# Optimization experiments

Hardware: AMD Instinct MI355X
Metric: run time of the kernel (lower is better)

The kernel has to match this reference:

```python
import jax, jax.numpy as jnp
import numpy as np

D = 256
H = 4
HD = D // H


def setup_inputs() -> dict:
    key = jax.random.key(0)
    ks = jax.random.split(key, 12)
    A, T = 64, 512
    s = 1.0 / np.sqrt(D)
    return {
        "features": jax.random.normal(ks[0], (A, T, D), jnp.float32),
        "positions": jax.random.normal(ks[1], (A, T, 2), jnp.float32),
        "Wq": jax.random.normal(ks[2], (D, D), jnp.float32) * s,
        "bq": jnp.zeros((D,), jnp.float32),
        "Wk": jax.random.normal(ks[3], (D, D), jnp.float32) * s,
        "bk": jnp.zeros((D,), jnp.float32),
        "Wv": jax.random.normal(ks[4], (D, D), jnp.float32) * s,
        "bv": jnp.zeros((D,), jnp.float32),
        "Wo": jax.random.normal(ks[5], (D, D), jnp.float32) * s,
        "bo": jnp.zeros((D,), jnp.float32),
        "max_distance": 2,
        "time_window": 64,
    }


def _sparse_mask(positions, max_distance, time_window):
    # positions: [A, T, 2] -> allowed [A, T, T]
    A, T, _ = positions.shape
    diff = positions[:, :, None, :] - positions[:, None, :, :]  # [A,T,T,2]
    dist2 = jnp.sum(diff * diff, axis=-1)                       # [A,T,T]
    t = jnp.arange(T)
    tmask = jnp.abs(t[:, None] - t[None, :]) <= time_window      # [T,T]
    return (dist2 <= float(max_distance) ** 2) & tmask[None]     # [A,T,T]


def reference(features, positions, Wq, bq, Wk, bk, Wv, bv, Wo, bo,
              max_distance, time_window):
    A, T, Dm = features.shape
    allowed = _sparse_mask(positions, max_distance, time_window)  # [A,T,T]
    q = features @ Wq.T + bq
    k = features @ Wk.T + bk
    v = features @ Wv.T + bv
    # split heads: [A, T, H, HD]
    q = q.reshape(A, T, H, HD)
    k = k.reshape(A, T, H, HD)
    v = v.reshape(A, T, H, HD)
    scale = 1.0 / np.sqrt(HD)
    scores = jnp.einsum("athd,ashd->ahts", q, k) * scale          # [A,H,T,T]
    scores = jnp.where(allowed[:, None], scores, -jnp.inf)
    attn = jax.nn.softmax(scores, axis=-1)
    out = jnp.einsum("ahts,ashd->athd", attn, v).reshape(A, T, Dm)
    return out @ Wo.T + bo
```

## Files before the change

### kernel.cpp

```cpp
#include <hip/hip_runtime.h>
#include <hip/hip_bf16.h>
#include <cstdint>
#include <cstddef>

typedef __attribute__((ext_vector_type(8))) _Float16 half8;
typedef __attribute__((ext_vector_type(4))) float floatx4;

#define MFMA16(a, b, c) __builtin_amdgcn_mfma_f32_16x16x32_f16((a), (b), (c), 0, 0, 0)

#define GLOAD_LDS16(g, l)                                                     \
    __builtin_amdgcn_global_load_lds(                                         \
        (const __attribute__((address_space(1))) void*)(g),                   \
        (__attribute__((address_space(3))) void*)(l), 16, 0, 0)

#define NFEAT 8388608

__global__ __launch_bounds__(256) void qkv_fused(
    const float* __restrict__ feat,
    const float* __restrict__ Wq, const float* __restrict__ Wk,
    const float* __restrict__ Wv,
    const float* __restrict__ bq, const float* __restrict__ bk,
    const float* __restrict__ bv,
    _Float16* __restrict__ Qb, _Float16* __restrict__ Kb, _Float16* __restrict__ Vb)
{
    __shared__ _Float16 Xs[4 * 128 * 64];
    __shared__ _Float16 Ws[128 * 64];

    const int n   = blockIdx.x;
    const int idx = n >> 3;
    const int bm  = (n & 7) * 32 + (idx >> 1);
    const int bn  = idx & 1;

    const int tid  = threadIdx.x;
    const int lane = tid & 63, wid = tid >> 6;
    const int quad = lane >> 4, l16 = lane & 15;
    const int wm = wid & 1, wn = wid >> 1;

    const float* Xg = feat + (size_t)bm * 128 * 256;
#pragma unroll
    for (int sl = 0; sl < 4; ++sl)
#pragma unroll
        for (int i = 0; i < 4; ++i) {
            int g   = tid + 256 * i;
            int row = g >> 3, chd = g & 7;
            int chs = chd ^ (row & 7);
            const float* s = Xg + (size_t)row * 256 + sl * 64 + chs * 8;
            float4 v0 = *(const float4*)s;
            float4 v1 = *(const float4*)(s + 4);
            half8 h = { (_Float16)v0.x, (_Float16)v0.y, (_Float16)v0.z, (_Float16)v0.w,
                        (_Float16)v1.x, (_Float16)v1.y, (_Float16)v1.z, (_Float16)v1.w };
            *(half8*)(&Xs[sl * 8192 + row * 64 + chd * 8]) = h;
        }

    const float* Wz[3] = { Wq, Wk, Wv };
    const float* bz[3] = { bq, bk, bv };
    _Float16*    oz[3] = { Qb, Kb, Vb };

    int wrow[4], wchd[4];
#pragma unroll
    for (int i = 0; i < 4; ++i) {
        int g = tid + 256 * i;
        wrow[i] = g >> 3;
        wchd[i] = g & 7;
    }
    float4 pv0[4], pv1[4];

    auto loadW = [&](int t) {
        const float* base = Wz[t >> 2] + (size_t)bn * 32768 + (t & 3) * 64;
#pragma unroll
        for (int i = 0; i < 4; ++i) {
            int chs = wchd[i] ^ (wrow[i] & 7);
            const float* s = base + (size_t)wrow[i] * 256 + chs * 8;
            pv0[i] = *(const float4*)s;
            pv1[i] = *(const float4*)(s + 4);
        }
    };
    auto storeW = [&]() {
#pragma unroll
        for (int i = 0; i < 4; ++i) {
            half8 h = { (_Float16)pv0[i].x, (_Float16)pv0[i].y,
                        (_Float16)pv0[i].z, (_Float16)pv0[i].w,
                        (_Float16)pv1[i].x, (_Float16)pv1[i].y,
                        (_Float16)pv1[i].z, (_Float16)pv1[i].w };
            *(half8*)(&Ws[wrow[i] * 64 + wchd[i] * 8]) = h;
        }
    };

    loadW(0);
    storeW();
    floatx4 acc[4][4] = {};

#pragma unroll 1
    for (int t = 0; t < 12; ++t) {
        __syncthreads();
        if (t < 11) loadW(t + 1);
        const int ks = t & 3;
#pragma unroll
        for (int kh = 0; kh < 2; ++kh) {
            half8 af[4], bf[4];
#pragma unroll
            for (int mi = 0; mi < 4; ++mi) {
                int row = wm * 64 + mi * 16 + l16;
                int cs  = (kh * 4 + quad) ^ (row & 7);
                af[mi] = *(const half8*)(&Xs[ks * 8192 + row * 64 + cs * 8]);
            }
#pragma unroll
            for (int ni = 0; ni < 4; ++ni) {
                int row = wn * 64 + ni * 16 + l16;
                int cs  = (kh * 4 + quad) ^ (row & 7);
                bf[ni] = *(const half8*)(&Ws[row * 64 + cs * 8]);
            }
#pragma unroll
            for (int mi = 0; mi < 4; ++mi)
#pragma unroll
                for (int ni = 0; ni < 4; ++ni)
                    acc[mi][ni] = MFMA16(af[mi], bf[ni], acc[mi][ni]);
        }
        __syncthreads();
        if (t < 11) storeW();
        if ((t & 3) == 3) {
            const int z = t >> 2;
            const float* bias = bz[z];
            _Float16*    outp = oz[z];
#pragma unroll
            for (int ni = 0; ni < 4; ++ni) {
                int col = bn * 128 + wn * 64 + ni * 16 + l16;
                float bv2 = bias[col];
#pragma unroll
                for (int mi = 0; mi < 4; ++mi) {
#pragma unroll
                    for (int r = 0; r < 4; ++r) {
                        int row = bm * 128 + wm * 64 + mi * 16 + quad * 4 + r;
                        outp[(size_t)row * 256 + col] =
                            (_Float16)(acc[mi][ni][r] + bv2);
                    }
                    acc[mi][ni] = floatx4{0.f, 0.f, 0.f, 0.f};
                }
            }
        }
    }
}

__global__ __launch_bounds__(256) void out_gemm(
    const _Float16* __restrict__ attnH, const float* __restrict__ Wo,
    const float* __restrict__ bo, float* __restrict__ out)
{
    __shared__ _Float16 Xs[4 * 128 * 64];
    __shared__ _Float16 Ws[128 * 64];

    const int n   = blockIdx.x;
    const int idx = n >> 3;
    const int bm  = (n & 7) * 32 + (idx >> 1);
    const int bn  = idx & 1;

    const int tid  = threadIdx.x;
    const int lane = tid & 63, wid = tid >> 6;
    const int quad = lane >> 4, l16 = lane & 15;
    const int wm = wid & 1, wn = wid >> 1;

    const _Float16* Ag = attnH + (size_t)bm * 128 * 256;
#pragma unroll
    for (int sl = 0; sl < 4; ++sl)
#pragma unroll
        for (int i = 0; i < 4; ++i) {
            int grp = wid * 4 + i;
            int row = grp * 8 + (lane >> 3);
            int sc  = (lane & 7) ^ (row & 7);
            GLOAD_LDS16(Ag + (size_t)row * 256 + sl * 64 + sc * 8,
                        Xs + sl * 8192 + grp * 512);
        }

    int wrow[4], wchd[4];
#pragma unroll
    for (int i = 0; i < 4; ++i) {
        int g = tid + 256 * i;
        wrow[i] = g >> 3;
        wchd[i] = g & 7;
    }
    float4 pv0[4], pv1[4];

    auto loadW = [&](int t) {
        const float* base = Wo + (size_t)bn * 32768 + t * 64;
#pragma unroll
        for (int i = 0; i < 4; ++i) {
            int chs = wchd[i] ^ (wrow[i] & 7);
            const float* s = base + (size_t)wrow[i] * 256 + chs * 8;
            pv0[i] = *(const float4*)s;
            pv1[i] = *(const float4*)(s + 4);
        }
    };
    auto storeW = [&]() {
#pragma unroll
        for (int i = 0; i < 4; ++i) {
            half8 h = { (_Float16)pv0[i].x, (_Float16)pv0[i].y,
                        (_Float16)pv0[i].z, (_Float16)pv0[i].w,
                        (_Float16)pv1[i].x, (_Float16)pv1[i].y,
                        (_Float16)pv1[i].z, (_Float16)pv1[i].w };
            *(half8*)(&Ws[wrow[i] * 64 + wchd[i] * 8]) = h;
        }
    };

    loadW(0);
    storeW();
    floatx4 acc[4][4] = {};

#pragma unroll 1
    for (int t = 0; t < 4; ++t) {
        __syncthreads();
        if (t < 3) loadW(t + 1);
#pragma unroll
        for (int kh = 0; kh < 2; ++kh) {
            half8 af[4], bf[4];
#pragma unroll
            for (int mi = 0; mi < 4; ++mi) {
                int row = wm * 64 + mi * 16 + l16;
                int cs  = (kh * 4 + quad) ^ (row & 7);
                af[mi] = *(const half8*)(&Xs[t * 8192 + row * 64 + cs * 8]);
            }
#pragma unroll
            for (int ni = 0; ni < 4; ++ni) {
                int row = wn * 64 + ni * 16 + l16;
                int cs  = (kh * 4 + quad) ^ (row & 7);
                bf[ni] = *(const half8*)(&Ws[row * 64 + cs * 8]);
            }
#pragma unroll
            for (int mi = 0; mi < 4; ++mi)
#pragma unroll
                for (int ni = 0; ni < 4; ++ni)
                    acc[mi][ni] = MFMA16(af[mi], bf[ni], acc[mi][ni]);
        }
        __syncthreads();
        if (t < 3) storeW();
    }

#pragma unroll
    for (int ni = 0; ni < 4; ++ni) {
        int col = bn * 128 + wn * 64 + ni * 16 + l16;
        float bv = bo[col];
#pragma unroll
        for (int mi = 0; mi < 4; ++mi)
#pragma unroll
            for (int r = 0; r < 4; ++r) {
                int row = bm * 128 + wm * 64 + mi * 16 + quad * 4 + r;
                out[(size_t)row * 256 + col] = acc[mi][ni][r] + bv;
            }
    }
}

__global__ __launch_bounds__(256) void attn_kernel(
    const _Float16* __restrict__ Qb, const _Float16* __restrict__ Kb,
    const _Float16* __restrict__ Vb, const float* __restrict__ positions,
    const int* __restrict__ mdp, const int* __restrict__ twp,
    _Float16* __restrict__ attnb)
{
    const int n   = blockIdx.x;
    const int idx = n >> 3;
    const int a   = (n & 7) * 8 + (idx >> 5);
    const int rem = idx & 31;
    const int qt  = rem >> 2, h = rem & 3;

    const int q0 = qt * 64;
    const int s_base = q0 - 64;
    const int tid = threadIdx.x, lane = tid & 63, wid = tid >> 6;
    const int quad = lane >> 4, l16 = lane & 15;

    __shared__ _Float16 KPs[192 * 64];
    __shared__ _Float16 Vt[64 * 192];

    const size_t abase = (size_t)a * 512;
    const int md = *mdp, tw = *twp;
    const float md2 = (float)(md * md);

    const size_t qrow = abase + q0 + wid * 16 + l16;
    half8 aq0 = *(const half8*)(Qb + qrow * 256 + h * 64 + quad * 8);
    half8 aq1 = *(const half8*)(Qb + qrow * 256 + h * 64 + 32 + quad * 8);
    float qpx[4], qpy[4];
    int trow[4];
#pragma unroll
    for (int r = 0; r < 4; ++r) {
        int m = wid * 16 + quad * 4 + r;
        trow[r] = q0 + m;
        float2 qp = *(const float2*)(positions + (abase + q0 + m) * 2);
        qpx[r] = qp.x;
        qpy[r] = qp.y;
    }

#pragma unroll
    for (int i = 0; i < 6; ++i) {
        int grp = wid * 6 + i;
        int si  = grp * 8 + (lane >> 3);
        int sc  = min(max(s_base + si, 0), 511);
        int ch  = (lane & 7) ^ (si & 7);
        GLOAD_LDS16(Kb + (abase + sc) * 256 + h * 64 + ch * 8, KPs + grp * 512);
    }
#pragma unroll
    for (int i = 0; i < 3; ++i) {
        int g   = tid + 256 * i;
        int si2 = (g % 96) * 2;
        int d0  = (g / 96) * 8;
        int sa  = min(max(s_base + si2, 0), 511);
        int sb  = min(max(s_base + si2 + 1, 0), 511);
        half8 v0 = *(const half8*)(Vb + (abase + sa) * 256 + h * 64 + d0);
        half8 v1 = *(const half8*)(Vb + (abase + sb) * 256 + h * 64 + d0);
        int c = si2 >> 3;
#pragma unroll
        for (int j = 0; j < 8; ++j) {
            int d  = d0 + j;
            int cs = (c & ~7) | ((c & 7) ^ (d & 7));
            union { _Float16 hh[2]; uint32_t u; } p;
            p.hh[0] = v0[j]; p.hh[1] = v1[j];
            *(uint32_t*)(&Vt[d * 192 + cs * 8 + (si2 & 7)]) = p.u;
        }
    }
    __syncthreads();

    floatx4 S[12];
#pragma unroll
    for (int j = 0; j < 12; ++j) {
        int si = j * 16 + l16;
        half8 bk0 = *(const half8*)(&KPs[si * 64 + ((quad) ^ (si & 7)) * 8]);
        half8 bk1 = *(const half8*)(&KPs[si * 64 + ((4 + quad) ^ (si & 7)) * 8]);
        floatx4 acc = {};
        acc = MFMA16(aq0, bk0, acc);
        acc = MFMA16(aq1, bk1, acc);
        int sr = s_base + si;
        int sc = min(max(sr, 0), 511);
        float2 kp = *(const float2*)(positions + (abase + sc) * 2);
        bool svalid = (sr >= 0) && (sr < 512);
#pragma unroll
        for (int r = 0; r < 4; ++r) {
            float dx = qpx[r] - kp.x, dy = qpy[r] - kp.y;
            float d2 = dx * dx + dy * dy;
            int dt = trow[r] - sr; dt = dt < 0 ? -dt : dt;
            bool ok = svalid && (d2 <= md2) && (dt <= tw);
            S[j][r] = ok ? acc[r] * 0.125f : -1e30f;
        }
    }

    float minv[4];
#pragma unroll
    for (int r = 0; r < 4; ++r) {
        float m = -1e30f;
#pragma unroll
        for (int j = 0; j < 12; ++j) m = fmaxf(m, S[j][r]);
        m = fmaxf(m, __shfl_xor(m, 1));
        m = fmaxf(m, __shfl_xor(m, 2));
        m = fmaxf(m, __shfl_xor(m, 4));
        m = fmaxf(m, __shfl_xor(m, 8));
        float l = 0.f;
#pragma unroll
        for (int j = 0; j < 12; ++j) {
            float p = __expf(S[j][r] - m);
            S[j][r] = p;
            l += p;
        }
        l += __shfl_xor(l, 1);
        l += __shfl_xor(l, 2);
        l += __shfl_xor(l, 4);
        l += __shfl_xor(l, 8);
        minv[r] = 1.0f / l;
    }

    __syncthreads();

    _Float16* Ps = KPs + wid * (16 * 192);
#pragma unroll
    for (int j = 0; j < 12; ++j)
#pragma unroll
        for (int r = 0; r < 4; ++r) {
            int row = quad * 4 + r;
            int col = j * 16 + l16;
            int ch  = (col >> 3) ^ (row & 7);
            Ps[row * 192 + ch * 8 + (col & 7)] = (_Float16)(S[j][r] * minv[r]);
        }

    half8 af[6];
#pragma unroll
    for (int k = 0; k < 6; ++k) {
        int ch = (k * 4 + quad) ^ (l16 & 7);
        af[k] = *(const half8*)(&Ps[l16 * 192 + ch * 8]);
    }
#pragma unroll
    for (int nn = 0; nn < 4; ++nn) {
        floatx4 accO = {};
#pragma unroll
        for (int k = 0; k < 6; ++k) {
            int row = nn * 16 + l16;
            int c   = k * 4 + quad;
            int cs  = (c & ~7) | ((c & 7) ^ (row & 7));
            half8 bv = *(const half8*)(&Vt[row * 192 + cs * 8]);
            accO = MFMA16(af[k], bv, accO);
        }
#pragma unroll
        for (int r = 0; r < 4; ++r) {
            int row = q0 + wid * 16 + quad * 4 + r;
            attnb[(abase + row) * 256 + h * 64 + nn * 16 + l16] = (_Float16)accO[r];
        }
    }
}

extern "C" void kernel_launch(void* const* d_in, const int* in_sizes, int n_in,
                              void* d_out, int out_size, void* d_ws, size_t ws_size,
                              hipStream_t stream)
{
    const float* feat = (const float*)d_in[0];
    const float* pos  = (const float*)d_in[1];
    const float* Wq   = (const float*)d_in[2];
    const float* bq   = (const float*)d_in[3];
    const float* Wk   = (const float*)d_in[4];
    const float* bk   = (const float*)d_in[5];
    const float* Wv   = (const float*)d_in[6];
    const float* bv   = (const float*)d_in[7];
    const float* Wo   = (const float*)d_in[8];
    const float* bo   = (const float*)d_in[9];
    const int*   md   = (const int*)d_in[10];
    const int*   tw   = (const int*)d_in[11];
    float*       out  = (float*)d_out;

    _Float16* ws    = (_Float16*)d_ws;
    _Float16* Qb    = ws;
    _Float16* Kb    = Qb + NFEAT;
    _Float16* Vb    = Kb + NFEAT;
    _Float16* attnH = Vb + NFEAT;

    qkv_fused<<<512, 256, 0, stream>>>(feat, Wq, Wk, Wv, bq, bk, bv, Qb, Kb, Vb);

    attn_kernel<<<2048, 256, 0, stream>>>(Qb, Kb, Vb, pos, md, tw, attnH);

    out_gemm<<<512, 256, 0, stream>>>(attnH, Wo, bo, out);
}
```

Measured before the change: 170.1 us.

## Fuse attention with output projection and pre-convert inputs to fp16

```diff
diff --git a/kernel.cpp b/kernel.cpp
--- a/kernel.cpp
+++ b/kernel.cpp
@@ -4,6 +4,7 @@
 #include <cstddef>
 
 typedef __attribute__((ext_vector_type(8))) _Float16 half8;
+typedef __attribute__((ext_vector_type(4))) _Float16 half4v;
 typedef __attribute__((ext_vector_type(4))) float floatx4;
 
 #define MFMA16(a, b, c) __builtin_amdgcn_mfma_f32_16x16x32_f16((a), (b), (c), 0, 0, 0)
@@ -14,11 +15,32 @@
         (__attribute__((address_space(3))) void*)(l), 16, 0, 0)
 
 #define NFEAT 8388608
+#define NW    65536
+
+__global__ __launch_bounds__(256) void convert_kernel(
+    const float* __restrict__ feat, const float* __restrict__ wq,
+    const float* __restrict__ wk, const float* __restrict__ wv,
+    const float* __restrict__ wo, _Float16* __restrict__ out)
+{
+    long tid  = (long)blockIdx.x * blockDim.x + threadIdx.x;
+    long base = tid * 4;
+    if (base >= (long)NFEAT + 4L * NW) return;
+    const float* src;
+    long off;
+    if (base < NFEAT) { src = feat; off = base; }
+    else {
+        long r = base - NFEAT;
+        int  w = (int)(r >> 16);
+        off = r & (NW - 1);
+        src = (w == 0) ? wq : (w == 1) ? wk : (w == 2) ? wv : wo;
+    }
+    float4 v = *(const float4*)(src + off);
+    half4v h = { (_Float16)v.x, (_Float16)v.y, (_Float16)v.z, (_Float16)v.w };
+    *(half4v*)(out + base) = h;
+}
 
 __global__ __launch_bounds__(256) void qkv_fused(
-    const float* __restrict__ feat,
-    const float* __restrict__ Wq, const float* __restrict__ Wk,
-    const float* __restrict__ Wv,
+    const _Float16* __restrict__ featH, const _Float16* __restrict__ WH,
     const float* __restrict__ bq, const float* __restrict__ bk,
     const float* __restrict__ bv,
     _Float16* __restrict__ Qb, _Float16* __restrict__ Kb, _Float16* __restrict__ Vb)
@@ -36,23 +58,18 @@
     const int quad = lane >> 4, l16 = lane & 15;
     const int wm = wid & 1, wn = wid >> 1;
 
-    const float* Xg = feat + (size_t)bm * 128 * 256;
+    const _Float16* Xg = featH + (size_t)bm * 128 * 256;
 #pragma unroll
     for (int sl = 0; sl < 4; ++sl)
 #pragma unroll
         for (int i = 0; i < 4; ++i) {
-            int g   = tid + 256 * i;
-            int row = g >> 3, chd = g & 7;
-            int chs = chd ^ (row & 7);
-            const float* s = Xg + (size_t)row * 256 + sl * 64 + chs * 8;
-            float4 v0 = *(const float4*)s;
-            float4 v1 = *(const float4*)(s + 4);
-            half8 h = { (_Float16)v0.x, (_Float16)v0.y, (_Float16)v0.z, (_Float16)v0.w,
-                        (_Float16)v1.x, (_Float16)v1.y, (_Float16)v1.z, (_Float16)v1.w };
-            *(half8*)(&Xs[sl * 8192 + row * 64 + chd * 8]) = h;
-        }
-
-    const float* Wz[3] = { Wq, Wk, Wv };
+            int grp = wid * 4 + i;
+            int row = grp * 8 + (lane >> 3);
+            int sc  = (lane & 7) ^ (row & 7);
+            GLOAD_LDS16(Xg + (size_t)row * 256 + sl * 64 + sc * 8,
+                        Xs + sl * 8192 + grp * 512);
+        }
+
     const float* bz[3] = { bq, bk, bv };
     _Float16*    oz[3] = { Qb, Kb, Vb };
 
@@ -63,27 +80,21 @@
         wrow[i] = g >> 3;
         wchd[i] = g & 7;
     }
-    float4 pv0[4], pv1[4];
+    half8 pw[4];
 
     auto loadW = [&](int t) {
-        const float* base = Wz[t >> 2] + (size_t)bn * 32768 + (t & 3) * 64;
+        const _Float16* base = WH + (size_t)(t >> 2) * NW
+                             + (size_t)bn * 32768 + (t & 3) * 64;
 #pragma unroll
         for (int i = 0; i < 4; ++i) {
             int chs = wchd[i] ^ (wrow[i] & 7);
-            const float* s = base + (size_t)wrow[i] * 256 + chs * 8;
-            pv0[i] = *(const float4*)s;
-            pv1[i] = *(const float4*)(s + 4);
+            pw[i] = *(const half8*)(base + (size_t)wrow[i] * 256 + chs * 8);
         }
     };
     auto storeW = [&]() {
 #pragma unroll
-        for (int i = 0; i < 4; ++i) {
-            half8 h = { (_Float16)pv0[i].x, (_Float16)pv0[i].y,
-                        (_Float16)pv0[i].z, (_Float16)pv0[i].w,
-                        (_Float16)pv1[i].x, (_Float16)pv1[i].y,
-                        (_Float16)pv1[i].z, (_Float16)pv1[i].w };
-            *(half8*)(&Ws[wrow[i] * 64 + wchd[i] * 8]) = h;
-        }
+        for (int i = 0; i < 4; ++i)
+            *(half8*)(&Ws[wrow[i] * 64 + wchd[i] * 8]) = pw[i];
     };
 
     loadW(0);
@@ -141,139 +152,34 @@
     }
 }
 
-__global__ __launch_bounds__(256) void out_gemm(
-    const _Float16* __restrict__ attnH, const float* __restrict__ Wo,
-    const float* __restrict__ bo, float* __restrict__ out)
+__global__ __launch_bounds__(256) void attn_out(
+    const _Float16* __restrict__ Qb, const _Float16* __restrict__ Kb,
+    const _Float16* __restrict__ Vb, const _Float16* __restrict__ WoH,
+    const float* __restrict__ positions, const float* __restrict__ bo,
+    const int* __restrict__ mdp, const int* __restrict__ twp,
+    float* __restrict__ out)
 {
-    __shared__ _Float16 Xs[4 * 128 * 64];
-    __shared__ _Float16 Ws[128 * 64];
+    __shared__ _Float16 SH[24576];
+    __shared__ _Float16 Wos[16384];
+
+    _Float16* KPs = SH;
+    _Float16* Vt  = SH + 12288;
+    _Float16* Os  = SH;
 
     const int n   = blockIdx.x;
     const int idx = n >> 3;
-    const int bm  = (n & 7) * 32 + (idx >> 1);
-    const int bn  = idx & 1;
-
-    const int tid  = threadIdx.x;
-    const int lane = tid & 63, wid = tid >> 6;
-    const int quad = lane >> 4, l16 = lane & 15;
-    const int wm = wid & 1, wn = wid >> 1;
-
-    const _Float16* Ag = attnH + (size_t)bm * 128 * 256;
-#pragma unroll
-    for (int sl = 0; sl < 4; ++sl)
-#pragma unroll
-        for (int i = 0; i < 4; ++i) {
-            int grp = wid * 4 + i;
-            int row = grp * 8 + (lane >> 3);
-            int sc  = (lane & 7) ^ (row & 7);
-            GLOAD_LDS16(Ag + (size_t)row * 256 + sl * 64 + sc * 8,
-                        Xs + sl * 8192 + grp * 512);
-        }
-
-    int wrow[4], wchd[4];
-#pragma unroll
-    for (int i = 0; i < 4; ++i) {
-        int g = tid + 256 * i;
-        wrow[i] = g >> 3;
-        wchd[i] = g & 7;
-    }
-    float4 pv0[4], pv1[4];
-
-    auto loadW = [&](int t) {
-        const float* base = Wo + (size_t)bn * 32768 + t * 64;
-#pragma unroll
-        for (int i = 0; i < 4; ++i) {
-            int chs = wchd[i] ^ (wrow[i] & 7);
-            const float* s = base + (size_t)wrow[i] * 256 + chs * 8;
-            pv0[i] = *(const float4*)s;
-            pv1[i] = *(const float4*)(s + 4);
-        }
-    };
-    auto storeW = [&]() {
-#pragma unroll
-        for (int i = 0; i < 4; ++i) {
-            half8 h = { (_Float16)pv0[i].x, (_Float16)pv0[i].y,
-                        (_Float16)pv0[i].z, (_Float16)pv0[i].w,
-                        (_Float16)pv1[i].x, (_Float16)pv1[i].y,
-                        (_Float16)pv1[i].z, (_Float16)pv1[i].w };
-            *(half8*)(&Ws[wrow[i] * 64 + wchd[i] * 8]) = h;
-        }
-    };
-
-    loadW(0);
-    storeW();
-    floatx4 acc[4][4] = {};
-
-#pragma unroll 1
-    for (int t = 0; t < 4; ++t) {
-        __syncthreads();
-        if (t < 3) loadW(t + 1);
-#pragma unroll
-        for (int kh = 0; kh < 2; ++kh) {
-            half8 af[4], bf[4];
-#pragma unroll
-            for (int mi = 0; mi < 4; ++mi) {
-                int row = wm * 64 + mi * 16 + l16;
-                int cs  = (kh * 4 + quad) ^ (row & 7);
-                af[mi] = *(const half8*)(&Xs[t * 8192 + row * 64 + cs * 8]);
-            }
-#pragma unroll
-            for (int ni = 0; ni < 4; ++ni) {
-                int row = wn * 64 + ni * 16 + l16;
-                int cs  = (kh * 4 + quad) ^ (row & 7);
-                bf[ni] = *(const half8*)(&Ws[row * 64 + cs * 8]);
-            }
-#pragma unroll
-            for (int mi = 0; mi < 4; ++mi)
-#pragma unroll
-                for (int ni = 0; ni < 4; ++ni)
-                    acc[mi][ni] = MFMA16(af[mi], bf[ni], acc[mi][ni]);
-        }
-        __syncthreads();
-        if (t < 3) storeW();
-    }
-
-#pragma unroll
-    for (int ni = 0; ni < 4; ++ni) {
-        int col = bn * 128 + wn * 64 + ni * 16 + l16;
-        float bv = bo[col];
-#pragma unroll
-        for (int mi = 0; mi < 4; ++mi)
-#pragma unroll
-            for (int r = 0; r < 4; ++r) {
-                int row = bm * 128 + wm * 64 + mi * 16 + quad * 4 + r;
-                out[(size_t)row * 256 + col] = acc[mi][ni][r] + bv;
-            }
-    }
-}
-
-__global__ __launch_bounds__(256) void attn_kernel(
-    const _Float16* __restrict__ Qb, const _Float16* __restrict__ Kb,
-    const _Float16* __restrict__ Vb, const float* __restrict__ positions,
-    const int* __restrict__ mdp, const int* __restrict__ twp,
-    _Float16* __restrict__ attnb)
-{
-    const int n   = blockIdx.x;
-    const int idx = n >> 3;
-    const int a   = (n & 7) * 8 + (idx >> 5);
-    const int rem = idx & 31;
-    const int qt  = rem >> 2, h = rem & 3;
+    const int a   = (n & 7) * 8 + (idx >> 3);
+    const int qt  = idx & 7;
 
     const int q0 = qt * 64;
     const int s_base = q0 - 64;
     const int tid = threadIdx.x, lane = tid & 63, wid = tid >> 6;
     const int quad = lane >> 4, l16 = lane & 15;
 
-    __shared__ _Float16 KPs[192 * 64];
-    __shared__ _Float16 Vt[64 * 192];
-
     const size_t abase = (size_t)a * 512;
     const int md = *mdp, tw = *twp;
     const float md2 = (float)(md * md);
 
-    const size_t qrow = abase + q0 + wid * 16 + l16;
-    half8 aq0 = *(const half8*)(Qb + qrow * 256 + h * 64 + quad * 8);
-    half8 aq1 = *(const half8*)(Qb + qrow * 256 + h * 64 + 32 + quad * 8);
     float qpx[4], qpy[4];
     int trow[4];
 #pragma unroll
@@ -284,45 +190,10 @@
         qpx[r] = qp.x;
         qpy[r] = qp.y;
     }
-
-#pragma unroll
-    for (int i = 0; i < 6; ++i) {
-        int grp = wid * 6 + i;
-        int si  = grp * 8 + (lane >> 3);
-        int sc  = min(max(s_base + si, 0), 511);
-        int ch  = (lane & 7) ^ (si & 7);
-        GLOAD_LDS16(Kb + (abase + sc) * 256 + h * 64 + ch * 8, KPs + grp * 512);
-    }
-#pragma unroll
-    for (int i = 0; i < 3; ++i) {
-        int g   = tid + 256 * i;
-        int si2 = (g % 96) * 2;
-        int d0  = (g / 96) * 8;
-        int sa  = min(max(s_base + si2, 0), 511);
-        int sb  = min(max(s_base + si2 + 1, 0), 511);
-        half8 v0 = *(const half8*)(Vb + (abase + sa) * 256 + h * 64 + d0);
-        half8 v1 = *(const half8*)(Vb + (abase + sb) * 256 + h * 64 + d0);
-        int c = si2 >> 3;
-#pragma unroll
-        for (int j = 0; j < 8; ++j) {
-            int d  = d0 + j;
-            int cs = (c & ~7) | ((c & 7) ^ (d & 7));
-            union { _Float16 hh[2]; uint32_t u; } p;
-            p.hh[0] = v0[j]; p.hh[1] = v1[j];
-            *(uint32_t*)(&Vt[d * 192 + cs * 8 + (si2 & 7)]) = p.u;
-        }
-    }
-    __syncthreads();
-
-    floatx4 S[12];
+    uint64_t ok_bits = 0;
 #pragma unroll
     for (int j = 0; j < 12; ++j) {
         int si = j * 16 + l16;
-        half8 bk0 = *(const half8*)(&KPs[si * 64 + ((quad) ^ (si & 7)) * 8]);
-        half8 bk1 = *(const half8*)(&KPs[si * 64 + ((4 + quad) ^ (si & 7)) * 8]);
-        floatx4 acc = {};
-        acc = MFMA16(aq0, bk0, acc);
-        acc = MFMA16(aq1, bk1, acc);
         int sr = s_base + si;
         int sc = min(max(sr, 0), 511);
         float2 kp = *(const float2*)(positions + (abase + sc) * 2);
@@ -332,69 +203,174 @@
             float dx = qpx[r] - kp.x, dy = qpy[r] - kp.y;
             float d2 = dx * dx + dy * dy;
             int dt = trow[r] - sr; dt = dt < 0 ? -dt : dt;
-            bool ok = svalid && (d2 <= md2) && (dt <= tw);
-            S[j][r] = ok ? acc[r] * 0.125f : -1e30f;
-        }
-    }
-
-    float minv[4];
-#pragma unroll
-    for (int r = 0; r < 4; ++r) {
-        float m = -1e30f;
-#pragma unroll
-        for (int j = 0; j < 12; ++j) m = fmaxf(m, S[j][r]);
-        m = fmaxf(m, __shfl_xor(m, 1));
-        m = fmaxf(m, __shfl_xor(m, 2));
-        m = fmaxf(m, __shfl_xor(m, 4));
-        m = fmaxf(m, __shfl_xor(m, 8));
-        float l = 0.f;
+            if (svalid && (d2 <= md2) && (dt <= tw))
+                ok_bits |= (1ull << (j * 4 + r));
+        }
+    }
+
+    floatx4 accO[4][4] = {};
+
+#pragma unroll
+    for (int h = 0; h < 4; ++h) {
+#pragma unroll
+        for (int i = 0; i < 6; ++i) {
+            int grp = wid * 6 + i;
+            int si  = grp * 8 + (lane >> 3);
+            int sc  = min(max(s_base + si, 0), 511);
+            int ch  = (lane & 7) ^ (si & 7);
+            GLOAD_LDS16(Kb + (abase + sc) * 256 + h * 64 + ch * 8, KPs + grp * 512);
+        }
+#pragma unroll
+        for (int i = 0; i < 3; ++i) {
+            int g   = tid + 256 * i;
+            int si2 = (g % 96) * 2;
+            int d0  = (g / 96) * 8;
+            int sa  = min(max(s_base + si2, 0), 511);
+            int sb  = min(max(s_base + si2 + 1, 0), 511);
+            half8 v0 = *(const half8*)(Vb + (abase + sa) * 256 + h * 64 + d0);
+            half8 v1 = *(const half8*)(Vb + (abase + sb) * 256 + h * 64 + d0);
+            int c = si2 >> 3;
+#pragma unroll
+            for (int j = 0; j < 8; ++j) {
+                int d  = d0 + j;
+                int cs = (c & ~7) | ((c & 7) ^ (d & 7));
+                union { _Float16 hh[2]; uint32_t u; } p;
+                p.hh[0] = v0[j]; p.hh[1] = v1[j];
+                *(uint32_t*)(&Vt[d * 192 + cs * 8 + (si2 & 7)]) = p.u;
+            }
+        }
+        const size_t qrow = abase + q0 + wid * 16 + l16;
+        half8 aq0 = *(const half8*)(Qb + qrow * 256 + h * 64 + quad * 8);
+        half8 aq1 = *(const half8*)(Qb + qrow * 256 + h * 64 + 32 + quad * 8);
+        __syncthreads();
+
+        floatx4 S[12];
 #pragma unroll
         for (int j = 0; j < 12; ++j) {
-            float p = __expf(S[j][r] - m);
-            S[j][r] = p;
-            l += p;
-        }
-        l += __shfl_xor(l, 1);
-        l += __shfl_xor(l, 2);
-        l += __shfl_xor(l, 4);
-        l += __shfl_xor(l, 8);
-        minv[r] = 1.0f / l;
-    }
-
-    __syncthreads();
-
-    _Float16* Ps = KPs + wid * (16 * 192);
-#pragma unroll
-    for (int j = 0; j < 12; ++j)
+            int si = j * 16 + l16;
+            half8 bk0 = *(const half8*)(&KPs[si * 64 + ((quad) ^ (si & 7)) * 8]);
+            half8 bk1 = *(const half8*)(&KPs[si * 64 + ((4 + quad) ^ (si & 7)) * 8]);
+            floatx4 acc = {};
+            acc = MFMA16(aq0, bk0, acc);
+            acc = MFMA16(aq1, bk1, acc);
+#pragma unroll
+            for (int r = 0; r < 4; ++r) {
+                bool ok = (ok_bits >> (j * 4 + r)) & 1;
+                S[j][r] = ok ? acc[r] * 0.125f : -1e30f;
+            }
+        }
+
+        float minv[4];
 #pragma unroll
         for (int r = 0; r < 4; ++r) {
-            int row = quad * 4 + r;
-            int col = j * 16 + l16;
-            int ch  = (col >> 3) ^ (row & 7);
-            Ps[row * 192 + ch * 8 + (col & 7)] = (_Float16)(S[j][r] * minv[r]);
-        }
-
-    half8 af[6];
-#pragma unroll
-    for (int k = 0; k < 6; ++k) {
-        int ch = (k * 4 + quad) ^ (l16 & 7);
-        af[k] = *(const half8*)(&Ps[l16 * 192 + ch * 8]);
-    }
-#pragma unroll
-    for (int nn = 0; nn < 4; ++nn) {
-        floatx4 accO = {};
+            float m = -1e30f;
+#pragma unroll
+            for (int j = 0; j < 12; ++j) m = fmaxf(m, S[j][r]);
+            m = fmaxf(m, __shfl_xor(m, 1));
+            m = fmaxf(m, __shfl_xor(m, 2));
+            m = fmaxf(m, __shfl_xor(m, 4));
+            m = fmaxf(m, __shfl_xor(m, 8));
+            float l = 0.f;
+#pragma unroll
+            for (int j = 0; j < 12; ++j) {
+                float p = __expf(S[j][r] - m);
+                S[j][r] = p;
+                l += p;
+            }
+            l += __shfl_xor(l, 1);
+            l += __shfl_xor(l, 2);
+            l += __shfl_xor(l, 4);
+            l += __shfl_xor(l, 8);
+            minv[r] = 1.0f / l;
+        }
+
+        __syncthreads();
+
+        _Float16* Ps = KPs + wid * (16 * 192);
+#pragma unroll
+        for (int j = 0; j < 12; ++j)
+#pragma unroll
+            for (int r = 0; r < 4; ++r) {
+                int row = quad * 4 + r;
+                int col = j * 16 + l16;
+                int ch  = (col >> 3) ^ (row & 7);
+                Ps[row * 192 + ch * 8 + (col & 7)] = (_Float16)(S[j][r] * minv[r]);
+            }
+
+        half8 af[6];
 #pragma unroll
         for (int k = 0; k < 6; ++k) {
-            int row = nn * 16 + l16;
-            int c   = k * 4 + quad;
+            int ch = (k * 4 + quad) ^ (l16 & 7);
+            af[k] = *(const half8*)(&Ps[l16 * 192 + ch * 8]);
+        }
+#pragma unroll
+        for (int nn = 0; nn < 4; ++nn) {
+#pragma unroll
+            for (int k = 0; k < 6; ++k) {
+                int row = nn * 16 + l16;
+                int c   = k * 4 + quad;
+                int cs  = (c & ~7) | ((c & 7) ^ (row & 7));
+                half8 bv = *(const half8*)(&Vt[row * 192 + cs * 8]);
+                accO[h][nn] = MFMA16(af[k], bv, accO[h][nn]);
+            }
+        }
+        __syncthreads();
+    }
+
+#pragma unroll
+    for (int h = 0; h < 4; ++h)
+#pragma unroll
+        for (int nn = 0; nn < 4; ++nn)
+#pragma unroll
+            for (int r = 0; r < 4; ++r) {
+                int row = wid * 16 + quad * 4 + r;
+                int col = h * 64 + nn * 16 + l16;
+                int c   = col >> 3;
+                int cs  = (c & ~7) | ((c & 7) ^ (row & 7));
+                Os[row * 256 + cs * 8 + (col & 7)] = (_Float16)accO[h][nn][r];
+            }
+
+    floatx4 accD[16] = {};
+#pragma unroll 1
+    for (int t = 0; t < 4; ++t) {
+        __syncthreads();
+#pragma unroll
+        for (int i = 0; i < 8; ++i) {
+            int grp = wid * 8 + i;
+            int row = grp * 8 + (lane >> 3);
+            int sc  = (lane & 7) ^ (row & 7);
+            GLOAD_LDS16(WoH + (size_t)row * 256 + t * 64 + sc * 8, Wos + grp * 512);
+        }
+        __syncthreads();
+
+        half8 af2[2];
+#pragma unroll
+        for (int kk = 0; kk < 2; ++kk) {
+            int row = wid * 16 + l16;
+            int c   = (t * 2 + kk) * 4 + quad;
             int cs  = (c & ~7) | ((c & 7) ^ (row & 7));
-            half8 bv = *(const half8*)(&Vt[row * 192 + cs * 8]);
-            accO = MFMA16(af[k], bv, accO);
-        }
+            af2[kk] = *(const half8*)(&Os[row * 256 + cs * 8]);
+        }
+#pragma unroll
+        for (int ni = 0; ni < 16; ++ni) {
+            int row = ni * 16 + l16;
+#pragma unroll
+            for (int kk = 0; kk < 2; ++kk) {
+                int cs = ((kk * 4 + quad)) ^ (row & 7);
+                half8 bf = *(const half8*)(&Wos[row * 64 + cs * 8]);
+                accD[ni] = MFMA16(af2[kk], bf, accD[ni]);
+            }
+        }
+    }
+
+#pragma unroll
+    for (int ni = 0; ni < 16; ++ni) {
+        int col = ni * 16 + l16;
+        float bv = bo[col];
 #pragma unroll
         for (int r = 0; r < 4; ++r) {
             int row = q0 + wid * 16 + quad * 4 + r;
-            attnb[(abase + row) * 256 + h * 64 + nn * 16 + l16] = (_Float16)accO[r];
+            out[(abase + row) * 256 + col] = accD[ni][r] + bv;
         }
     }
 }
@@ -418,14 +394,16 @@
     float*       out  = (float*)d_out;
 
     _Float16* ws    = (_Float16*)d_ws;
-    _Float16* Qb    = ws;
+    _Float16* featH = ws;
+    _Float16* WH    = featH + NFEAT;
+    _Float16* WoHp  = WH + 3 * (size_t)NW;
+    _Float16* Qb    = WH + 4 * (size_t)NW;
     _Float16* Kb    = Qb + NFEAT;
     _Float16* Vb    = Kb + NFEAT;
-    _Float16* attnH = Vb + NFEAT;
-
-    qkv_fused<<<512, 256, 0, stream>>>(feat, Wq, Wk, Wv, bq, bk, bv, Qb, Kb, Vb);
-
-    attn_kernel<<<2048, 256, 0, stream>>>(Qb, Kb, Vb, pos, md, tw, attnH);
-
-    out_gemm<<<512, 256, 0, stream>>>(attnH, Wo, bo, out);
+
+    convert_kernel<<<8448, 256, 0, stream>>>(feat, Wq, Wk, Wv, Wo, ws);
+
+    qkv_fused<<<512, 256, 0, stream>>>(featH, WH, bq, bk, bv, Qb, Kb, Vb);
+
+    attn_out<<<512, 256, 0, stream>>>(Qb, Kb, Vb, WoHp, pos, bo, md, tw, out);
 }
```

After: 186.1 us. +9.4%, slower.

## Pre-convert inputs to fp16, precompute sparse mask bits, drop softmax max

Applied to the files above, without the earlier changes.

```diff
diff --git a/kernel.cpp b/kernel.cpp
--- a/kernel.cpp
+++ b/kernel.cpp
@@ -4,6 +4,7 @@
 #include <cstddef>
 
 typedef __attribute__((ext_vector_type(8))) _Float16 half8;
+typedef __attribute__((ext_vector_type(4))) _Float16 half4v;
 typedef __attribute__((ext_vector_type(4))) float floatx4;
 
 #define MFMA16(a, b, c) __builtin_amdgcn_mfma_f32_16x16x32_f16((a), (b), (c), 0, 0, 0)
@@ -14,11 +15,75 @@
         (__attribute__((address_space(3))) void*)(l), 16, 0, 0)
 
 #define NFEAT 8388608
+#define NW    65536
+#define NCVT  8448
+
+__global__ __launch_bounds__(256) void convert_kernel(
+    const float* __restrict__ feat, const float* __restrict__ wq,
+    const float* __restrict__ wk, const float* __restrict__ wv,
+    const float* __restrict__ wo, const float* __restrict__ positions,
+    const int* __restrict__ mdp, const int* __restrict__ twp,
+    _Float16* __restrict__ out, uint64_t* __restrict__ maskbuf)
+{
+    if (blockIdx.x >= NCVT) {
+        const int n2 = blockIdx.x - NCVT;
+        const int a = n2 >> 3, qt = n2 & 7;
+        const int q0 = qt * 64, s_base = q0 - 64;
+        const int tid = threadIdx.x, lane = tid & 63, wid = tid >> 6;
+        const int quad = lane >> 4, l16 = lane & 15;
+        const size_t abase = (size_t)a * 512;
+        const int md = *mdp, tw = *twp;
+        const float md2 = (float)(md * md);
+
+        float qpx[4], qpy[4];
+        int trow[4];
+#pragma unroll
+        for (int r = 0; r < 4; ++r) {
+            int m = wid * 16 + quad * 4 + r;
+            trow[r] = q0 + m;
+            float2 qp = *(const float2*)(positions + (abase + q0 + m) * 2);
+            qpx[r] = qp.x;
+            qpy[r] = qp.y;
+        }
+        uint64_t ok_bits = 0;
+#pragma unroll
+        for (int j = 0; j < 12; ++j) {
+            int si = j * 16 + l16;
+            int sr = s_base + si;
+            int sc = min(max(sr, 0), 511);
+            float2 kp = *(const float2*)(positions + (abase + sc) * 2);
+            bool svalid = (sr >= 0) && (sr < 512);
+#pragma unroll
+            for (int r = 0; r < 4; ++r) {
+                float dx = qpx[r] - kp.x, dy = qpy[r] - kp.y;
+                float d2 = dx * dx + dy * dy;
+                int dt = trow[r] - sr; dt = dt < 0 ? -dt : dt;
+                if (svalid && (d2 <= md2) && (dt <= tw))
+                    ok_bits |= (1ull << (j * 4 + r));
+            }
+        }
+        maskbuf[(size_t)n2 * 256 + tid] = ok_bits;
+        return;
+    }
+
+    long tid  = (long)blockIdx.x * blockDim.x + threadIdx.x;
+    long base = tid * 4;
+    const float* src;
+    long off;
+    if (base < NFEAT) { src = feat; off = base; }
+    else {
+        long r = base - NFEAT;
+        int  w = (int)(r >> 16);
+        off = r & (NW - 1);
+        src = (w == 0) ? wq : (w == 1) ? wk : (w == 2) ? wv : wo;
+    }
+    float4 v = *(const float4*)(src + off);
+    half4v h = { (_Float16)v.x, (_Float16)v.y, (_Float16)v.z, (_Float16)v.w };
+    *(half4v*)(out + base) = h;
+}
 
 __global__ __launch_bounds__(256) void qkv_fused(
-    const float* __restrict__ feat,
-    const float* __restrict__ Wq, const float* __restrict__ Wk,
-    const float* __restrict__ Wv,
+    const _Float16* __restrict__ featH, const _Float16* __restrict__ WH,
     const float* __restrict__ bq, const float* __restrict__ bk,
     const float* __restrict__ bv,
     _Float16* __restrict__ Qb, _Float16* __restrict__ Kb, _Float16* __restrict__ Vb)
@@ -36,26 +101,6 @@
     const int quad = lane >> 4, l16 = lane & 15;
     const int wm = wid & 1, wn = wid >> 1;
 
-    const float* Xg = feat + (size_t)bm * 128 * 256;
-#pragma unroll
-    for (int sl = 0; sl < 4; ++sl)
-#pragma unroll
-        for (int i = 0; i < 4; ++i) {
-            int g   = tid + 256 * i;
-            int row = g >> 3, chd = g & 7;
-            int chs = chd ^ (row & 7);
-            const float* s = Xg + (size_t)row * 256 + sl * 64 + chs * 8;
-            float4 v0 = *(const float4*)s;
-            float4 v1 = *(const float4*)(s + 4);
-            half8 h = { (_Float16)v0.x, (_Float16)v0.y, (_Float16)v0.z, (_Float16)v0.w,
-                        (_Float16)v1.x, (_Float16)v1.y, (_Float16)v1.z, (_Float16)v1.w };
-            *(half8*)(&Xs[sl * 8192 + row * 64 + chd * 8]) = h;
-        }
-
-    const float* Wz[3] = { Wq, Wk, Wv };
-    const float* bz[3] = { bq, bk, bv };
-    _Float16*    oz[3] = { Qb, Kb, Vb };
-
     int wrow[4], wchd[4];
 #pragma unroll
     for (int i = 0; i < 4; ++i) {
@@ -63,30 +108,39 @@
         wrow[i] = g >> 3;
         wchd[i] = g & 7;
     }
-    float4 pv0[4], pv1[4];
-
+    half8 pw[4];
     auto loadW = [&](int t) {
-        const float* base = Wz[t >> 2] + (size_t)bn * 32768 + (t & 3) * 64;
+        const _Float16* base = WH + (size_t)(t >> 2) * NW
+                             + (size_t)bn * 32768 + (t & 3) * 64;
 #pragma unroll
         for (int i = 0; i < 4; ++i) {
             int chs = wchd[i] ^ (wrow[i] & 7);
-            const float* s = base + (size_t)wrow[i] * 256 + chs * 8;
-            pv0[i] = *(const float4*)s;
-            pv1[i] = *(const float4*)(s + 4);
+            pw[i] = *(const half8*)(base + (size_t)wrow[i] * 256 + chs * 8);
         }
     };
     auto storeW = [&]() {
 #pragma unroll
+        for (int i = 0; i < 4; ++i)
+            *(half8*)(&Ws[wrow[i] * 64 + wchd[i] * 8]) = pw[i];
+    };
+
+    loadW(0);
+
+    const _Float16* Xg = featH + (size_t)bm * 128 * 256;
+#pragma unroll
+    for (int sl = 0; sl < 4; ++sl)
+#pragma unroll
         for (int i = 0; i < 4; ++i) {
-            half8 h = { (_Float16)pv0[i].x, (_Float16)pv0[i].y,
-                        (_Float16)pv0[i].z, (_Float16)pv0[i].w,
-                        (_Float16)pv1[i].x, (_Float16)pv1[i].y,
-                        (_Float16)pv1[i].z, (_Float16)pv1[i].w };
-            *(half8*)(&Ws[wrow[i] * 64 + wchd[i] * 8]) = h;
-        }
-    };
-
-    loadW(0);
+            int grp = wid * 4 + i;
+            int row = grp * 8 + (lane >> 3);
+            int sc  = (lane & 7) ^ (row & 7);
+            GLOAD_LDS16(Xg + (size_t)row * 256 + sl * 64 + sc * 8,
+                        Xs + sl * 8192 + grp * 512);
+        }
+
+    const float* bz[3] = { bq, bk, bv };
+    _Float16*    oz[3] = { Qb, Kb, Vb };
+
     storeW();
     floatx4 acc[4][4] = {};
 
@@ -141,116 +195,9 @@
     }
 }
 
-__global__ __launch_bounds__(256) void out_gemm(
-    const _Float16* __restrict__ attnH, const float* __restrict__ Wo,
-    const float* __restrict__ bo, float* __restrict__ out)
-{
-    __shared__ _Float16 Xs[4 * 128 * 64];
-    __shared__ _Float16 Ws[128 * 64];
-
-    const int n   = blockIdx.x;
-    const int idx = n >> 3;
-    const int bm  = (n & 7) * 32 + (idx >> 1);
-    const int bn  = idx & 1;
-
-    const int tid  = threadIdx.x;
-    const int lane = tid & 63, wid = tid >> 6;
-    const int quad = lane >> 4, l16 = lane & 15;
-    const int wm = wid & 1, wn = wid >> 1;
-
-    const _Float16* Ag = attnH + (size_t)bm * 128 * 256;
-#pragma unroll
-    for (int sl = 0; sl < 4; ++sl)
-#pragma unroll
-        for (int i = 0; i < 4; ++i) {
-            int grp = wid * 4 + i;
-            int row = grp * 8 + (lane >> 3);
-            int sc  = (lane & 7) ^ (row & 7);
-            GLOAD_LDS16(Ag + (size_t)row * 256 + sl * 64 + sc * 8,
-                        Xs + sl * 8192 + grp * 512);
-        }
-
-    int wrow[4], wchd[4];
-#pragma unroll
-    for (int i = 0; i < 4; ++i) {
-        int g = tid + 256 * i;
-        wrow[i] = g >> 3;
-        wchd[i] = g & 7;
-    }
-    float4 pv0[4], pv1[4];
-
-    auto loadW = [&](int t) {
-        const float* base = Wo + (size_t)bn * 32768 + t * 64;
-#pragma unroll
-        for (int i = 0; i < 4; ++i) {
-            int chs = wchd[i] ^ (wrow[i] & 7);
-            const float* s = base + (size_t)wrow[i] * 256 + chs * 8;
-            pv0[i] = *(const float4*)s;
-            pv1[i] = *(const float4*)(s + 4);
-        }
-    };
-    auto storeW = [&]() {
-#pragma unroll
-        for (int i = 0; i < 4; ++i) {
-            half8 h = { (_Float16)pv0[i].x, (_Float16)pv0[i].y,
-                        (_Float16)pv0[i].z, (_Float16)pv0[i].w,
-                        (_Float16)pv1[i].x, (_Float16)pv1[i].y,
-                        (_Float16)pv1[i].z, (_Float16)pv1[i].w };
-            *(half8*)(&Ws[wrow[i] * 64 + wchd[i] * 8]) = h;
-        }
-    };
-
-    loadW(0);
-    storeW();
-    floatx4 acc[4][4] = {};
-
-#pragma unroll 1
-    for (int t = 0; t < 4; ++t) {
-        __syncthreads();
-        if (t < 3) loadW(t + 1);
-#pragma unroll
-        for (int kh = 0; kh < 2; ++kh) {
-            half8 af[4], bf[4];
-#pragma unroll
-            for (int mi = 0; mi < 4; ++mi) {
-                int row = wm * 64 + mi * 16 + l16;
-                int cs  = (kh * 4 + quad) ^ (row & 7);
-                af[mi] = *(const half8*)(&Xs[t * 8192 + row * 64 + cs * 8]);
-            }
-#pragma unroll
-            for (int ni = 0; ni < 4; ++ni) {
-                int row = wn * 64 + ni * 16 + l16;
-                int cs  = (kh * 4 + quad) ^ (row & 7);
-                bf[ni] = *(const half8*)(&Ws[row * 64 + cs * 8]);
-            }
-#pragma unroll
-            for (int mi = 0; mi < 4; ++mi)
-#pragma unroll
-                for (int ni = 0; ni < 4; ++ni)
-                    acc[mi][ni] = MFMA16(af[mi], bf[ni], acc[mi][ni]);
-        }
-        __syncthreads();
-        if (t < 3) storeW();
-    }
-
-#pragma unroll
-    for (int ni = 0; ni < 4; ++ni) {
-        int col = bn * 128 + wn * 64 + ni * 16 + l16;
-        float bv = bo[col];
-#pragma unroll
-        for (int mi = 0; mi < 4; ++mi)
-#pragma unroll
-            for (int r = 0; r < 4; ++r) {
-                int row = bm * 128 + wm * 64 + mi * 16 + quad * 4 + r;
-                out[(size_t)row * 256 + col] = acc[mi][ni][r] + bv;
-            }
-    }
-}
-
 __global__ __launch_bounds__(256) void attn_kernel(
     const _Float16* __restrict__ Qb, const _Float16* __restrict__ Kb,
-    const _Float16* __restrict__ Vb, const float* __restrict__ positions,
-    const int* __restrict__ mdp, const int* __restrict__ twp,
+    const _Float16* __restrict__ Vb, const uint64_t* __restrict__ maskbuf,
     _Float16* __restrict__ attnb)
 {
     const int n   = blockIdx.x;
@@ -268,22 +215,12 @@
     __shared__ _Float16 Vt[64 * 192];
 
     const size_t abase = (size_t)a * 512;
-    const int md = *mdp, tw = *twp;
-    const float md2 = (float)(md * md);
+
+    const uint64_t ok_bits = maskbuf[(size_t)(a * 8 + qt) * 256 + tid];
 
     const size_t qrow = abase + q0 + wid * 16 + l16;
     half8 aq0 = *(const half8*)(Qb + qrow * 256 + h * 64 + quad * 8);
     half8 aq1 = *(const half8*)(Qb + qrow * 256 + h * 64 + 32 + quad * 8);
-    float qpx[4], qpy[4];
-    int trow[4];
-#pragma unroll
-    for (int r = 0; r < 4; ++r) {
-        int m = wid * 16 + quad * 4 + r;
-        trow[r] = q0 + m;
-        float2 qp = *(const float2*)(positions + (abase + q0 + m) * 2);
-        qpx[r] = qp.x;
-        qpy[r] = qp.y;
-    }
 
 #pragma unroll
     for (int i = 0; i < 6; ++i) {
@@ -323,37 +260,19 @@
         floatx4 acc = {};
         acc = MFMA16(aq0, bk0, acc);
         acc = MFMA16(aq1, bk1, acc);
-        int sr = s_base + si;
-        int sc = min(max(sr, 0), 511);
-        float2 kp = *(const float2*)(positions + (abase + sc) * 2);
-        bool svalid = (sr >= 0) && (sr < 512);
 #pragma unroll
         for (int r = 0; r < 4; ++r) {
-            float dx = qpx[r] - kp.x, dy = qpy[r] - kp.y;
-            float d2 = dx * dx + dy * dy;
-            int dt = trow[r] - sr; dt = dt < 0 ? -dt : dt;
-            bool ok = svalid && (d2 <= md2) && (dt <= tw);
-            S[j][r] = ok ? acc[r] * 0.125f : -1e30f;
+            bool ok = (ok_bits >> (j * 4 + r)) & 1;
+            S[j][r] = __expf(ok ? acc[r] * 0.125f : -1e30f);
         }
     }
 
     float minv[4];
 #pragma unroll
     for (int r = 0; r < 4; ++r) {
-        float m = -1e30f;
-#pragma unroll
-        for (int j = 0; j < 12; ++j) m = fmaxf(m, S[j][r]);
-        m = fmaxf(m, __shfl_xor(m, 1));
-        m = fmaxf(m, __shfl_xor(m, 2));
-        m = fmaxf(m, __shfl_xor(m, 4));
-        m = fmaxf(m, __shfl_xor(m, 8));
         float l = 0.f;
 #pragma unroll
-        for (int j = 0; j < 12; ++j) {
-            float p = __expf(S[j][r] - m);
-            S[j][r] = p;
-            l += p;
-        }
+        for (int j = 0; j < 12; ++j) l += S[j][r];
         l += __shfl_xor(l, 1);
         l += __shfl_xor(l, 2);
         l += __shfl_xor(l, 4);
@@ -396,6 +315,105 @@
             int row = q0 + wid * 16 + quad * 4 + r;
             attnb[(abase + row) * 256 + h * 64 + nn * 16 + l16] = (_Float16)accO[r];
         }
+    }
+}
+
+__global__ __launch_bounds__(256) void out_gemm(
+    const _Float16* __restrict__ attnH, const _Float16* __restrict__ WoH,
+    const float* __restrict__ bo, float* __restrict__ out)
+{
+    __shared__ _Float16 Xs[4 * 128 * 64];
+    __shared__ _Float16 Ws[128 * 64];
+
+    const int n   = blockIdx.x;
+    const int idx = n >> 3;
+    const int bm  = (n & 7) * 32 + (idx >> 1);
+    const int bn  = idx & 1;
+
+    const int tid  = threadIdx.x;
+    const int lane = tid & 63, wid = tid >> 6;
+    const int quad = lane >> 4, l16 = lane & 15;
+    const int wm = wid & 1, wn = wid >> 1;
+
+    int wrow[4], wchd[4];
+#pragma unroll
+    for (int i = 0; i < 4; ++i) {
+        int g = tid + 256 * i;
+        wrow[i] = g >> 3;
+        wchd[i] = g & 7;
+    }
+    half8 pw[4];
+    auto loadW = [&](int t) {
+        const _Float16* base = WoH + (size_t)bn * 32768 + t * 64;
+#pragma unroll
+        for (int i = 0; i < 4; ++i) {
+            int chs = wchd[i] ^ (wrow[i] & 7);
+            pw[i] = *(const half8*)(base + (size_t)wrow[i] * 256 + chs * 8);
+        }
+    };
+    auto storeW = [&]() {
+#pragma unroll
+        for (int i = 0; i < 4; ++i)
+            *(half8*)(&Ws[wrow[i] * 64 + wchd[i] * 8]) = pw[i];
+    };
+
+    loadW(0);
+
+    const _Float16* Ag = attnH + (size_t)bm * 128 * 256;
+#pragma unroll
+    for (int sl = 0; sl < 4; ++sl)
+#pragma unroll
+        for (int i = 0; i < 4; ++i) {
+            int grp = wid * 4 + i;
+            int row = grp * 8 + (lane >> 3);
+            int sc  = (lane & 7) ^ (row & 7);
+            GLOAD_LDS16(Ag + (size_t)row * 256 + sl * 64 + sc * 8,
+                        Xs + sl * 8192 + grp * 512);
+        }
+
+    storeW();
+    floatx4 acc[4][4] = {};
+
+#pragma unroll 1
+    for (int t = 0; t < 4; ++t) {
+        __syncthreads();
+        if (t < 3) loadW(t + 1);
+#pragma unroll
+        for (int kh = 0; kh < 2; ++kh) {
+            half8 af[4], bf[4];
+#pragma unroll
+            for (int mi = 0; mi < 4; ++mi) {
+                int row = wm * 64 + mi * 16 + l16;
+                int cs  = (kh * 4 + quad) ^ (row & 7);
+                af[mi] = *(const half8*)(&Xs[t * 8192 + row * 64 + cs * 8]);
+            }
+#pragma unroll
+            for (int ni = 0; ni < 4; ++ni) {
+                int row = wn * 64 + ni * 16 + l16;
+                int cs  = (kh * 4 + quad) ^ (row & 7);
+                bf[ni] = *(const half8*)(&Ws[row * 64 + cs * 8]);
+            }
+#pragma unroll
+            for (int mi = 0; mi < 4; ++mi)
+#pragma unroll
+                for (int ni = 0; ni < 4; ++ni)
+                    acc[mi][ni] = MFMA16(af[mi], bf[ni], acc[mi][ni]);
+        }
+        __syncthreads();
+        if (t < 3) storeW();
+    }
+
+#pragma unroll
+    for (int ni = 0; ni < 4; ++ni) {
+        int col = bn * 128 + wn * 64 + ni * 16 + l16;
+        float bv = bo[col];
+#pragma unroll
+        for (int mi = 0; mi < 4; ++mi)
+#pragma unroll
+            for (int r = 0; r < 4; ++r) {
+                int row = bm * 128 + wm * 64 + mi * 16 + quad * 4 + r;
+                out[(size_t)row * 256 + col] = acc[mi][ni][r] + bv;
+            }
     }
 }
 
@@ -418,14 +436,21 @@
     float*       out  = (float*)d_out;
 
     _Float16* ws    = (_Float16*)d_ws;
-    _Float16* Qb    = ws;
+    _Float16* featH = ws;
+    _Float16* WH    = featH + NFEAT;
+    _Float16* WoHp  = WH + 3 * (size_t)NW;
+    _Float16* Qb    = WH + 4 * (size_t)NW;
     _Float16* Kb    = Qb + NFEAT;
     _Float16* Vb    = Kb + NFEAT;
     _Float16* attnH = Vb + NFEAT;
-
-    qkv_fused<<<512, 256, 0, stream>>>(feat, Wq, Wk, Wv, bq, bk, bv, Qb, Kb, Vb);
-
-    attn_kernel<<<2048, 256, 0, stream>>>(Qb, Kb, Vb, pos, md, tw, attnH);
-
-    out_gemm<<<512, 256, 0, stream>>>(attnH, Wo, bo, out);
+    uint64_t* maskb = (uint64_t*)(attnH + NFEAT);
+
+    convert_kernel<<<NCVT + 512, 256, 0, stream>>>(
+        feat, Wq, Wk, Wv, Wo, pos, md, tw, ws, maskb);
+
+    qkv_fused<<<512, 256, 0, stream>>>(featH, WH, bq, bk, bv, Qb, Kb, Vb);
+
+    attn_kernel<<<2048, 256, 0, stream>>>(Qb, Kb, Vb, maskb, attnH);
+
+    out_gemm<<<512, 256, 0, stream>>>(attnH, WoHp, bo, out);
 }
```

Measured after the change: 169.2 us. About the same (-0.6%).
